# Kernel tuning notes

Hardware: AMD Instinct MI355X
Metric: run time of the kernel (lower is better)

The kernel has to match this reference:

```python
import jax, jax.numpy as jnp
import numpy as np

HID = 32
R = 3
B = 2
IN = 64
N = 100000
E = 1600000
G = 256


def setup_inputs() -> dict:
    key = jax.random.key(0)
    ks = jax.random.split(key, 16)
    x = jax.random.normal(ks[0], (N, IN), dtype=jnp.float32)
    src = jax.random.randint(ks[1], (E,), 0, N)
    dst = jax.random.randint(ks[2], (E,), 0, N)
    etype = jax.random.randint(ks[3], (E,), 0, R)
    graph_ids = jnp.sort(jax.random.randint(ks[4], (N,), 0, G))
    s = 0.05
    basis1 = jax.random.normal(ks[5], (B, IN, HID), dtype=jnp.float32) * s   # layer 1 basis
    basis_r = jax.random.normal(ks[6], (3, B, HID, HID), dtype=jnp.float32) * s  # layers 2-4
    w_comp = jax.random.normal(ks[7], (4, R, B), dtype=jnp.float32) * s     # per-layer basis coeffs
    loop1 = jax.random.normal(ks[8], (IN, HID), dtype=jnp.float32) * s
    loop_r = jax.random.normal(ks[9], (3, HID, HID), dtype=jnp.float32) * s
    bias = jnp.zeros((4, HID), dtype=jnp.float32)
    lin1_w = jax.random.normal(ks[10], (4 * HID, 64), dtype=jnp.float32) * s
    lin1_b = jnp.zeros((64,), dtype=jnp.float32)
    lin2_w = jax.random.normal(ks[11], (64, 1), dtype=jnp.float32) * s
    lin2_b = jnp.zeros((1,), dtype=jnp.float32)
    return dict(x=x, basis1=basis1, basis_r=basis_r, w_comp=w_comp, loop1=loop1,
                loop_r=loop_r, bias=bias, lin1_w=lin1_w, lin1_b=lin1_b,
                lin2_w=lin2_w, lin2_b=lin2_b, src=src, dst=dst, etype=etype,
                graph_ids=graph_ids, num_graphs=G)


def _rel_conv(h, basis, comp, loop_w, b, src, dst, etype, n_nodes):
    # basis-decomposed relation weights: W[r] = sum_b comp[r,b] * basis[b]
    W = jnp.einsum('rb,bio->rio', comp, basis)            # [R, in, out]
    h_rel = jnp.einsum('ni,rio->rno', h, W)               # [R, N, out]
    msg = h_rel[etype, src]                               # [E, out] edge-typed gather
    agg = jax.ops.segment_sum(msg, dst, num_segments=n_nodes)
    return agg + h @ loop_w + b                           # self-loop + bias


def reference(x, basis1, basis_r, w_comp, loop1, loop_r, bias,
              lin1_w, lin1_b, lin2_w, lin2_b,
              src, dst, etype, graph_ids, num_graphs):
    n = x.shape[0]
    h = jnp.tanh(_rel_conv(x, basis1, w_comp[0], loop1, bias[0], src, dst, etype, n))
    states = [h]
    for i in range(3):
        h = jnp.tanh(_rel_conv(h, basis_r[i], w_comp[i + 1], loop_r[i], bias[i + 1],
                               src, dst, etype, n))
        states.append(h)
    feat = jnp.concatenate(states, axis=1)                # [N, 128]
    # mean-pool nodes per graph (diff_pooling ~ dgl mean_nodes)
    summed = jax.ops.segment_sum(feat, graph_ids, num_segments=num_graphs)
    counts = jax.ops.segment_sum(jnp.ones((n,), feat.dtype), graph_ids,
                                 num_segments=num_graphs)
    pooled = summed / jnp.maximum(counts, 1.0)[:, None]   # [G, 128]
    hdn = jax.nn.relu(pooled @ lin1_w + lin1_b)
    out = jax.nn.sigmoid(hdn @ lin2_w + lin2_b)
    return out[:, 0]
```

## Files before the change

### kernel.cpp

```cpp
#include <hip/hip_runtime.h>
#include <cstdint>
#include <cmath>

#define DLO_BITS 7
#define DLO_MASK 127
#define SCAT_Q 2048

__global__ __launch_bounds__(256) void prep_w(
    const float* __restrict__ basis1,
    const float* __restrict__ w_comp,
    const float* __restrict__ loop1,
    float* __restrict__ W)
{
    int tid = blockIdx.x * 256 + threadIdx.x;
    if (tid < 8192) {
        int m = tid >> 11, io = tid & 2047;
        W[tid] = (m < 3)
            ? w_comp[m * 2] * basis1[io] + w_comp[m * 2 + 1] * basis1[2048 + io]
            : loop1[io];
    }
}

__global__ __launch_bounds__(256) void count_kernel(
    const int* __restrict__ dst, int* __restrict__ bcnt, int E, int NB)
{
    __shared__ int cnt[1024];
    for (int i = threadIdx.x; i < NB; i += 256) cnt[i] = 0;
    __syncthreads();
    int base = blockIdx.x * SCAT_Q;
    #pragma unroll
    for (int i = 0; i < SCAT_Q / 256; ++i) {
        int e = base + i * 256 + threadIdx.x;
        if (e < E) atomicAdd(&cnt[dst[e] >> DLO_BITS], 1);
    }
    __syncthreads();
    for (int i = threadIdx.x; i < NB; i += 256)
        if (cnt[i]) atomicAdd(&bcnt[i], cnt[i]);
}

__global__ __launch_bounds__(1024) void scan_kernel(
    const int* __restrict__ bcnt, int* __restrict__ bbase,
    int* __restrict__ bcur, int NB)
{
    __shared__ int s[1024];
    int t = threadIdx.x;
    int v = (t < NB) ? bcnt[t] : 0;
    s[t] = v; __syncthreads();
    for (int off = 1; off < 1024; off <<= 1) {
        int u = (t >= off) ? s[t - off] : 0;
        __syncthreads();
        s[t] += u;
        __syncthreads();
    }
    if (t < NB) { int b = s[t] - v; bbase[t] = b; bcur[t] = b; }
}

__global__ __launch_bounds__(256) void bscatter_kernel(
    const int* __restrict__ src, const int* __restrict__ dst,
    const int* __restrict__ et, int* __restrict__ bcur,
    unsigned* __restrict__ eidx1, int E, int NB)
{
    __shared__ int cnt[1024];
    __shared__ int bbs[1024];
    int tid = threadIdx.x;
    for (int i = tid; i < NB; i += 256) cnt[i] = 0;
    __syncthreads();
    int base = blockIdx.x * SCAT_Q;
    int lim = E - base; if (lim > SCAT_Q) lim = SCAT_Q;
    for (int i = tid; i < lim; i += 256)
        atomicAdd(&cnt[dst[base + i] >> DLO_BITS], 1);
    __syncthreads();
    for (int i = tid; i < NB; i += 256) {
        int c = cnt[i];
        bbs[i] = c ? atomicAdd(&bcur[i], c) : 0;
    }
    __syncthreads();
    for (int i = tid; i < NB; i += 256) cnt[i] = 0;
    __syncthreads();
    for (int i = tid; i < lim; i += 256) {
        int e = base + i;
        int d = dst[e];
        int bk = d >> DLO_BITS;
        int p = bbs[bk] + atomicAdd(&cnt[bk], 1);
        eidx1[p] = (unsigned)src[e] | ((unsigned)et[e] << 17)
                 | ((unsigned)(d & DLO_MASK) << 19);
    }
}

__global__ __launch_bounds__(256) void bucket_sort_kernel(
    const unsigned* __restrict__ eidx1, const int* __restrict__ bbase,
    const int* __restrict__ bcnt, unsigned* __restrict__ eidx2,
    int* __restrict__ rp, int* __restrict__ rend0, int* __restrict__ rend1,
    int* __restrict__ rend, int N)
{
    __shared__ int c512[512], excl[512], w[512];
    int tid = threadIdx.x, b = blockIdx.x;
    int gbase = bbase[b], cnt = bcnt[b], n0 = b << DLO_BITS;
    c512[tid] = 0; c512[tid + 256] = 0;
    __syncthreads();
    for (int k = tid; k < cnt; k += 256) {
        unsigned pk = eidx1[gbase + k];
        int key = (((pk >> 19) & DLO_MASK) << 2) | ((pk >> 17) & 3);
        atomicAdd(&c512[key], 1);
    }
    __syncthreads();
    w[tid] = c512[tid]; w[tid + 256] = c512[tid + 256];
    __syncthreads();
    for (int off = 1; off < 512; off <<= 1) {
        int a1 = (tid >= off) ? w[tid - off] : 0;
        int a2 = (tid + 256 >= off) ? w[tid + 256 - off] : 0;
        __syncthreads();
        w[tid] += a1; w[tid + 256] += a2;
        __syncthreads();
    }
    excl[tid] = w[tid] - c512[tid];
    excl[tid + 256] = w[tid + 256] - c512[tid + 256];
    __syncthreads();
    if (tid < 128) {
        int n = n0 + tid;
        if (n < N) {
            int k0 = tid << 2;
            rp[n]    = gbase + excl[k0];
            rend0[n] = gbase + excl[k0 | 1];
            rend1[n] = gbase + excl[k0 | 2];
            rend[n]  = gbase + excl[k0 | 2] + c512[k0 | 2];
        }
    }
    __syncthreads();
    c512[tid] = 0; c512[tid + 256] = 0;
    __syncthreads();
    for (int k = tid; k < cnt; k += 256) {
        unsigned pk = eidx1[gbase + k];
        int key = (((pk >> 19) & DLO_MASK) << 2) | ((pk >> 17) & 3);
        int p = excl[key] + atomicAdd(&c512[key], 1);
        eidx2[gbase + p] = pk;
    }
}

__global__ __launch_bounds__(256) void dense_kernel(
    const float* __restrict__ x,
    const float* __restrict__ W,
    const float* __restrict__ bias_l,
    float* __restrict__ hrel,
    float* __restrict__ agg,
    int N)
{
    __shared__ float sW[4 * 2048];
    __shared__ float sH[64 * 68];
    const int tid = threadIdx.x;
    for (int i = tid; i < 4 * 2048; i += 256) sW[i] = W[i];
    const int nb = blockIdx.x * 64;
    for (int idx = tid; idx < 64 * 64; idx += 256) {
        int n = idx >> 6, i = idx & 63;
        int gn = nb + n;
        sH[n * 68 + i] = (gn < N) ? x[(size_t)gn * 64 + i] : 0.0f;
    }
    __syncthreads();

    const int m  = tid >> 6;
    const int l  = tid & 63;
    const int ow = l & 7;
    const int ng = l >> 3;

    float acc[8][4];
    #pragma unroll
    for (int j = 0; j < 8; ++j)
        #pragma unroll
        for (int k = 0; k < 4; ++k) acc[j][k] = 0.0f;

    const float* wb = &sW[m * 2048 + ow * 4];
    #pragma unroll 2
    for (int i = 0; i < 64; i += 4) {
        float4 wv0 = *(const float4*)(wb + (i + 0) * 32);
        float4 wv1 = *(const float4*)(wb + (i + 1) * 32);
        float4 wv2 = *(const float4*)(wb + (i + 2) * 32);
        float4 wv3 = *(const float4*)(wb + (i + 3) * 32);
        #pragma unroll
        for (int j = 0; j < 8; ++j) {
            float4 hv = *(const float4*)&sH[(j * 8 + ng) * 68 + i];
            acc[j][0] += hv.x * wv0.x + hv.y * wv1.x + hv.z * wv2.x + hv.w * wv3.x;
            acc[j][1] += hv.x * wv0.y + hv.y * wv1.y + hv.z * wv2.y + hv.w * wv3.y;
            acc[j][2] += hv.x * wv0.z + hv.y * wv1.z + hv.z * wv2.z + hv.w * wv3.z;
            acc[j][3] += hv.x * wv0.w + hv.y * wv1.w + hv.z * wv2.w + hv.w * wv3.w;
        }
    }

    if (m < 3) {
        #pragma unroll
        for (int j = 0; j < 8; ++j) {
            int n = nb + j * 8 + ng;
            if (n < N)
                *(float4*)&hrel[((size_t)m * N + n) * 32 + ow * 4] =
                    make_float4(acc[j][0], acc[j][1], acc[j][2], acc[j][3]);
        }
    } else {
        float4 bb = *(const float4*)&bias_l[ow * 4];
        #pragma unroll
        for (int j = 0; j < 8; ++j) {
            int n = nb + j * 8 + ng;
            if (n < N)
                *(float4*)&agg[(size_t)n * 32 + ow * 4] =
                    make_float4(acc[j][0] + bb.x, acc[j][1] + bb.y,
                                acc[j][2] + bb.z, acc[j][3] + bb.w);
        }
    }
}

__global__ __launch_bounds__(256) void gather1_kernel(
    const unsigned* __restrict__ eidx, const int* __restrict__ rp,
    const int* __restrict__ rend0, const int* __restrict__ rend1,
    const int* __restrict__ rend,
    const float* __restrict__ hrel, const float* __restrict__ agg,
    float* __restrict__ feat, int N)
{
    int tid = blockIdx.x * 256 + threadIdx.x;
    int n = tid >> 3;
    if (n >= N) return;
    int c = (tid & 7) << 2;
    int e0 = rp[n], e1 = rend0[n], e2 = rend1[n], e3 = rend[n];
    const float4 bv = *(const float4*)&agg[(size_t)n * 32 + c];
    float ax = bv.x, ay = bv.y, az = bv.z, aw = bv.w;
    float bx = 0, by = 0, bz = 0, bw = 0;
    #pragma unroll
    for (int seg = 0; seg < 3; ++seg) {
        int ks = (seg == 0) ? e0 : ((seg == 1) ? e1 : e2);
        int ke = (seg == 0) ? e1 : ((seg == 1) ? e2 : e3);
        const float* hb = hrel + (size_t)seg * N * 32 + c;
        int k = ks;
        for (; k + 2 <= ke; k += 2) {
            unsigned p0 = eidx[k], p1 = eidx[k + 1];
            float4 v0 = *(const float4*)&hb[(size_t)(p0 & 0x1FFFF) * 32];
            float4 v1 = *(const float4*)&hb[(size_t)(p1 & 0x1FFFF) * 32];
            ax += v0.x; ay += v0.y; az += v0.z; aw += v0.w;
            bx += v1.x; by += v1.y; bz += v1.z; bw += v1.w;
        }
        if (k < ke) {
            unsigned p = eidx[k];
            float4 v = *(const float4*)&hb[(size_t)(p & 0x1FFFF) * 32];
            ax += v.x; ay += v.y; az += v.z; aw += v.w;
        }
    }
    float4* out = (float4*)&feat[(size_t)n * 128 + c];
    *out = make_float4(tanhf(ax + bx), tanhf(ay + by), tanhf(az + bz), tanhf(aw + bw));
}

__global__ __launch_bounds__(256) void fused_layer_kernel(
    const unsigned* __restrict__ eidx, const int* __restrict__ rp,
    const int* __restrict__ rend0, const int* __restrict__ rend1,
    const int* __restrict__ rend,
    const float* __restrict__ basis_b,
    const float* __restrict__ loop_w,
    const float* __restrict__ bias_l,
    const float* __restrict__ comp,
    const float* __restrict__ feat_in,
    float* __restrict__ feat_out,
    int N)
{
    __shared__ float sB0[1024], sB1[1024], sL[1024];
    __shared__ float sT0[32 * 36], sT1[32 * 36], sH[32 * 36];
    const int tid = threadIdx.x;
    for (int i = tid; i < 1024; i += 256) {
        sB0[i] = basis_b[i];
        sB1[i] = basis_b[1024 + i];
        sL[i]  = loop_w[i];
    }
    const int nn = tid >> 3, cg = (tid & 7) << 2;
    const int n = blockIdx.x * 32 + nn;

    float4 h4 = *(const float4*)&feat_in[(size_t)n * 128 + cg];
    *(float4*)&sH[nn * 36 + cg] = h4;

    int e0 = rp[n], e1 = rend0[n], e2 = rend1[n], e3 = rend[n];
    float t0x = 0, t0y = 0, t0z = 0, t0w = 0;
    float t1x = 0, t1y = 0, t1z = 0, t1w = 0;
    #pragma unroll
    for (int seg = 0; seg < 3; ++seg) {
        int ks = (seg == 0) ? e0 : ((seg == 1) ? e1 : e2);
        int ke = (seg == 0) ? e1 : ((seg == 1) ? e2 : e3);
        float sx = 0, sy = 0, sz = 0, sw = 0;
        float ux = 0, uy = 0, uz = 0, uw = 0;
        int k = ks;
        for (; k + 2 <= ke; k += 2) {
            unsigned p0 = eidx[k], p1 = eidx[k + 1];
            float4 v0 = *(const float4*)&feat_in[(size_t)(p0 & 0x1FFFF) * 128 + cg];
            float4 v1 = *(const float4*)&feat_in[(size_t)(p1 & 0x1FFFF) * 128 + cg];
            sx += v0.x; sy += v0.y; sz += v0.z; sw += v0.w;
            ux += v1.x; uy += v1.y; uz += v1.z; uw += v1.w;
        }
        if (k < ke) {
            unsigned p = eidx[k];
            float4 v = *(const float4*)&feat_in[(size_t)(p & 0x1FFFF) * 128 + cg];
            sx += v.x; sy += v.y; sz += v.z; sw += v.w;
        }
        sx += ux; sy += uy; sz += uz; sw += uw;
        float c0 = comp[seg * 2], c1 = comp[seg * 2 + 1];
        t0x += c0 * sx; t0y += c0 * sy; t0z += c0 * sz; t0w += c0 * sw;
        t1x += c1 * sx; t1y += c1 * sy; t1z += c1 * sz; t1w += c1 * sw;
    }
    *(float4*)&sT0[nn * 36 + cg] = make_float4(t0x, t0y, t0z, t0w);
    *(float4*)&sT1[nn * 36 + cg] = make_float4(t1x, t1y, t1z, t1w);
    __syncthreads();

    float4 bb = *(const float4*)&bias_l[cg];
    float a[4] = {bb.x, bb.y, bb.z, bb.w};
    #pragma unroll 8
    for (int kk = 0; kk < 32; ++kk) {
        float p0 = sT0[nn * 36 + kk];
        float p1 = sT1[nn * 36 + kk];
        float hh = sH[nn * 36 + kk];
        float4 b0 = *(const float4*)&sB0[kk * 32 + cg];
        float4 b1 = *(const float4*)&sB1[kk * 32 + cg];
        float4 lw = *(const float4*)&sL[kk * 32 + cg];
        a[0] += p0 * b0.x + p1 * b1.x + hh * lw.x;
        a[1] += p0 * b0.y + p1 * b1.y + hh * lw.y;
        a[2] += p0 * b0.z + p1 * b1.z + hh * lw.z;
        a[3] += p0 * b0.w + p1 * b1.w + hh * lw.w;
    }
    *(float4*)&feat_out[(size_t)n * 128 + cg] =
        make_float4(tanhf(a[0]), tanhf(a[1]), tanhf(a[2]), tanhf(a[3]));
}

__global__ __launch_bounds__(256) void pool_kernel(
    const float* __restrict__ feat, const int* __restrict__ gid,
    float* __restrict__ pooled, float* __restrict__ cntArr, int N)
{
    int chunk0 = blockIdx.x * 128;
    int ch = threadIdx.x & 127, half = threadIdx.x >> 7;
    int n = chunk0 + half;
    int lim = chunk0 + 128; if (lim > N) lim = N;
    if (n >= lim) return;
    int cur = gid[n];
    float acc = 0.0f; int cc = 0;
    for (; n < lim; n += 2) {
        int g = gid[n];
        if (g != cur) {
            atomicAdd(&pooled[(size_t)cur * 128 + ch], acc);
            if (ch == 0) atomicAdd(&cntArr[cur], (float)cc);
            acc = 0.0f; cc = 0; cur = g;
        }
        acc += feat[(size_t)n * 128 + ch];
        ++cc;
    }
    atomicAdd(&pooled[(size_t)cur * 128 + ch], acc);
    if (ch == 0) atomicAdd(&cntArr[cur], (float)cc);
}

__global__ __launch_bounds__(64) void mlp_kernel(
    const float* __restrict__ pooled, const float* __restrict__ cntArr,
    const float* __restrict__ w1, const float* __restrict__ b1,
    const float* __restrict__ w2, const float* __restrict__ b2,
    float* __restrict__ out)
{
    int g = blockIdx.x;
    int t = threadIdx.x;
    float inv = 1.0f / fmaxf(cntArr[g], 1.0f);
    float acc = b1[t];
    #pragma unroll 8
    for (int k = 0; k < 128; ++k)
        acc += pooled[(size_t)g * 128 + k] * inv * w1[k * 64 + t];
    float h = fmaxf(acc, 0.0f);
    float p = h * w2[t];
    #pragma unroll
    for (int off = 32; off > 0; off >>= 1) p += __shfl_down(p, off, 64);
    if (t == 0) out[g] = 1.0f / (1.0f + expf(-(p + b2[0])));
}

extern "C" void kernel_launch(void* const* d_in, const int* in_sizes, int n_in,
                              void* d_out, int out_size, void* d_ws, size_t ws_size,
                              hipStream_t stream)
{
    const float* x       = (const float*)d_in[0];
    const float* basis1  = (const float*)d_in[1];
    const float* basis_r = (const float*)d_in[2];
    const float* w_comp  = (const float*)d_in[3];
    const float* loop1   = (const float*)d_in[4];
    const float* loop_r  = (const float*)d_in[5];
    const float* bias    = (const float*)d_in[6];
    const float* lin1_w  = (const float*)d_in[7];
    const float* lin1_b  = (const float*)d_in[8];
    const float* lin2_w  = (const float*)d_in[9];
    const float* lin2_b  = (const float*)d_in[10];
    const int*   src     = (const int*)d_in[11];
    const int*   dst     = (const int*)d_in[12];
    const int*   etype   = (const int*)d_in[13];
    const int*   gid     = (const int*)d_in[14];

    const int N = in_sizes[0] / 64;
    const int E = in_sizes[11];
    const int G = out_size;
    const int NB = (N + DLO_MASK) >> DLO_BITS;

    float* ws      = (float*)d_ws;
    float* W       = ws;
    float* hrel    = W + 8192;
    float* agg     = hrel + (size_t)3 * N * 32;
    float* feat    = agg + (size_t)N * 32;
    float* pooled  = feat + (size_t)N * 128;
    float* cntArr  = pooled + (size_t)G * 128;
    int*   bcnt    = (int*)(cntArr + G);
    int*   bbase   = bcnt + NB;
    int*   bcur    = bbase + NB;
    int*   rp      = bcur + NB;
    int*   rend0   = rp + N;
    int*   rend1   = rend0 + N;
    int*   rend    = rend1 + N;
    unsigned* eidx2 = (unsigned*)(rend + N);
    unsigned* eidx1 = (unsigned*)feat;

    hipMemsetAsync(pooled, 0, ((size_t)G * 128 + G + NB) * sizeof(float), stream);
    prep_w<<<32, 256, 0, stream>>>(basis1, w_comp, loop1, W);

    const int nsb = (E + SCAT_Q - 1) / SCAT_Q;
    count_kernel<<<nsb, 256, 0, stream>>>(dst, bcnt, E, NB);
    scan_kernel<<<1, 1024, 0, stream>>>(bcnt, bbase, bcur, NB);
    bscatter_kernel<<<nsb, 256, 0, stream>>>(src, dst, etype, bcur, eidx1, E, NB);
    bucket_sort_kernel<<<NB, 256, 0, stream>>>(eidx1, bbase, bcnt, eidx2,
                                               rp, rend0, rend1, rend, N);

    dense_kernel<<<(N + 63) / 64, 256, 0, stream>>>(x, W, bias, hrel, agg, N);
    gather1_kernel<<<(N * 8 + 255) / 256, 256, 0, stream>>>(
        eidx2, rp, rend0, rend1, rend, hrel, agg, feat, N);

    for (int l = 1; l < 4; ++l) {
        fused_layer_kernel<<<(N + 31) / 32, 256, 0, stream>>>(
            eidx2, rp, rend0, rend1, rend,
            basis_r + (size_t)(l - 1) * 2048,
            loop_r + (size_t)(l - 1) * 1024,
            bias + l * 32,
            w_comp + l * 6,
            feat + (l - 1) * 32,
            feat + l * 32,
            N);
    }

    pool_kernel<<<(N + 127) / 128, 256, 0, stream>>>(feat, gid, pooled, cntArr, N);
    mlp_kernel<<<G, 64, 0, stream>>>(pooled, cntArr, lin1_w, lin1_b, lin2_w, lin2_b, (float*)d_out);
}
```

Before: 360.0 us.

## Replace count+scatter passes with single-pass chunk-local partition and start table

Merges the separate count and global-scatter kernels into one partition kernel. Each block sorts a 4096-edge chunk by bucket in shared memory, writes it contiguously, and records per-chunk bucket start offsets. The bucket sort kernel then gathers each bucket's segments from all chunks using a prefix sum and a binary search. This removes one full pass over the edge arrays and the scattered global writes. In exchange it adds a per-element binary search and scattered reads in the bucket sort.

```diff
diff --git a/kernel.cpp b/kernel.cpp
--- a/kernel.cpp
+++ b/kernel.cpp
@@ -4,7 +4,7 @@
 
 #define DLO_BITS 7
 #define DLO_MASK 127
-#define SCAT_Q 2048
+#define CHUNK 4096
 
 __global__ __launch_bounds__(256) void prep_w(
     const float* __restrict__ basis1,
@@ -21,26 +21,63 @@
     }
 }
 
-__global__ __launch_bounds__(256) void count_kernel(
-    const int* __restrict__ dst, int* __restrict__ bcnt, int E, int NB)
-{
+__global__ __launch_bounds__(256) void part_kernel(
+    const int* __restrict__ src, const int* __restrict__ dst,
+    const int* __restrict__ et, unsigned* __restrict__ eidx1,
+    int* __restrict__ startTab,
+    int* __restrict__ bcnt,
+    int E, int NB)
+{
+    __shared__ unsigned rec[CHUNK];
     __shared__ int cnt[1024];
-    for (int i = threadIdx.x; i < NB; i += 256) cnt[i] = 0;
-    __syncthreads();
-    int base = blockIdx.x * SCAT_Q;
-    #pragma unroll
-    for (int i = 0; i < SCAT_Q / 256; ++i) {
-        int e = base + i * 256 + threadIdx.x;
-        if (e < E) atomicAdd(&cnt[dst[e] >> DLO_BITS], 1);
-    }
-    __syncthreads();
-    for (int i = threadIdx.x; i < NB; i += 256)
-        if (cnt[i]) atomicAdd(&bcnt[i], cnt[i]);
+    __shared__ int w[1024];
+    const int tid = threadIdx.x;
+    const int base = blockIdx.x * CHUNK;
+    int lim = E - base; if (lim > CHUNK) lim = CHUNK;
+
+    cnt[tid] = 0; cnt[tid + 256] = 0; cnt[tid + 512] = 0; cnt[tid + 768] = 0;
+    __syncthreads();
+    for (int i = tid; i < lim; i += 256) {
+        int e = base + i;
+        int d = dst[e];
+        rec[i] = (unsigned)src[e] | ((unsigned)et[e] << 17)
+               | ((unsigned)(d & DLO_MASK) << 19);
+        atomicAdd(&cnt[d >> DLO_BITS], 1);
+    }
+    __syncthreads();
+    w[tid] = cnt[tid]; w[tid + 256] = cnt[tid + 256];
+    w[tid + 512] = cnt[tid + 512]; w[tid + 768] = cnt[tid + 768];
+    __syncthreads();
+    for (int off = 1; off < 1024; off <<= 1) {
+        int a0 = (tid >= off) ? w[tid - off] : 0;
+        int a1 = (tid + 256 >= off) ? w[tid + 256 - off] : 0;
+        int a2 = (tid + 512 >= off) ? w[tid + 512 - off] : 0;
+        int a3 = w[tid + 768 - off];
+        __syncthreads();
+        w[tid] += a0; w[tid + 256] += a1; w[tid + 512] += a2; w[tid + 768] += a3;
+        __syncthreads();
+    }
+    int* st = startTab + blockIdx.x * (NB + 1);
+    for (int bk = tid; bk < NB; bk += 256) {
+        int c = cnt[bk];
+        int ex = w[bk] - c;
+        st[bk] = base + ex;
+        w[bk] = ex;
+        if (c) atomicAdd(&bcnt[bk], c);
+    }
+    if (tid == 0) st[NB] = base + lim;
+    __syncthreads();
+    cnt[tid] = 0; cnt[tid + 256] = 0; cnt[tid + 512] = 0; cnt[tid + 768] = 0;
+    __syncthreads();
+    for (int i = tid; i < lim; i += 256) {
+        int bk = dst[base + i] >> DLO_BITS;
+        int pos = w[bk] + atomicAdd(&cnt[bk], 1);
+        eidx1[base + pos] = rec[i];
+    }
 }
 
 __global__ __launch_bounds__(1024) void scan_kernel(
-    const int* __restrict__ bcnt, int* __restrict__ bbase,
-    int* __restrict__ bcur, int NB)
+    const int* __restrict__ bcnt, int* __restrict__ bbase, int NB)
 {
     __shared__ int s[1024];
     int t = threadIdx.x;
@@ -52,72 +89,63 @@
         s[t] += u;
         __syncthreads();
     }
-    if (t < NB) { int b = s[t] - v; bbase[t] = b; bcur[t] = b; }
-}
-
-__global__ __launch_bounds__(256) void bscatter_kernel(
-    const int* __restrict__ src, const int* __restrict__ dst,
-    const int* __restrict__ et, int* __restrict__ bcur,
-    unsigned* __restrict__ eidx1, int E, int NB)
-{
-    __shared__ int cnt[1024];
-    __shared__ int bbs[1024];
-    int tid = threadIdx.x;
-    for (int i = tid; i < NB; i += 256) cnt[i] = 0;
-    __syncthreads();
-    int base = blockIdx.x * SCAT_Q;
-    int lim = E - base; if (lim > SCAT_Q) lim = SCAT_Q;
-    for (int i = tid; i < lim; i += 256)
-        atomicAdd(&cnt[dst[base + i] >> DLO_BITS], 1);
-    __syncthreads();
-    for (int i = tid; i < NB; i += 256) {
-        int c = cnt[i];
-        bbs[i] = c ? atomicAdd(&bcur[i], c) : 0;
-    }
-    __syncthreads();
-    for (int i = tid; i < NB; i += 256) cnt[i] = 0;
-    __syncthreads();
-    for (int i = tid; i < lim; i += 256) {
-        int e = base + i;
-        int d = dst[e];
-        int bk = d >> DLO_BITS;
-        int p = bbs[bk] + atomicAdd(&cnt[bk], 1);
-        eidx1[p] = (unsigned)src[e] | ((unsigned)et[e] << 17)
-                 | ((unsigned)(d & DLO_MASK) << 19);
-    }
+    if (t < NB) bbase[t] = s[t] - v;
 }
 
 __global__ __launch_bounds__(256) void bucket_sort_kernel(
-    const unsigned* __restrict__ eidx1, const int* __restrict__ bbase,
-    const int* __restrict__ bcnt, unsigned* __restrict__ eidx2,
+    const unsigned* __restrict__ eidx1, const int* __restrict__ startTab,
+    const int* __restrict__ bbase, unsigned* __restrict__ eidx2,
     int* __restrict__ rp, int* __restrict__ rend0, int* __restrict__ rend1,
-    int* __restrict__ rend, int N)
-{
-    __shared__ int c512[512], excl[512], w[512];
-    int tid = threadIdx.x, b = blockIdx.x;
-    int gbase = bbase[b], cnt = bcnt[b], n0 = b << DLO_BITS;
+    int* __restrict__ rend, int N, int NCH, int NB)
+{
+    __shared__ int rbase[512];
+    __shared__ int racc[512];
+    __shared__ int c512[512], excl[512], w2[512];
+    const int tid = threadIdx.x, b = blockIdx.x;
+
+    for (int j = tid; j < 512; j += 256) {
+        int s = 0, len = 0;
+        if (j < NCH) {
+            s = startTab[j * (NB + 1) + b];
+            len = startTab[j * (NB + 1) + b + 1] - s;
+        }
+        rbase[j] = s;
+        racc[j] = len;
+    }
+    __syncthreads();
+    for (int off = 1; off < 512; off <<= 1) {
+        int a1 = (tid >= off) ? racc[tid - off] : 0;
+        int a2 = (tid + 256 >= off) ? racc[tid + 256 - off] : 0;
+        __syncthreads();
+        racc[tid] += a1; racc[tid + 256] += a2;
+        __syncthreads();
+    }
+    const int cnt = racc[NCH - 1];
+    const int gbase = bbase[b];
     c512[tid] = 0; c512[tid + 256] = 0;
     __syncthreads();
-    for (int k = tid; k < cnt; k += 256) {
-        unsigned pk = eidx1[gbase + k];
+    for (int i = tid; i < cnt; i += 256) {
+        int lo = 0, hi = NCH - 1;
+        while (lo < hi) { int mid = (lo + hi) >> 1; if (racc[mid] <= i) lo = mid + 1; else hi = mid; }
+        unsigned pk = eidx1[rbase[lo] + (i - (lo ? racc[lo - 1] : 0))];
         int key = (((pk >> 19) & DLO_MASK) << 2) | ((pk >> 17) & 3);
         atomicAdd(&c512[key], 1);
     }
     __syncthreads();
-    w[tid] = c512[tid]; w[tid + 256] = c512[tid + 256];
+    w2[tid] = c512[tid]; w2[tid + 256] = c512[tid + 256];
     __syncthreads();
     for (int off = 1; off < 512; off <<= 1) {
-        int a1 = (tid >= off) ? w[tid - off] : 0;
-        int a2 = (tid + 256 >= off) ? w[tid + 256 - off] : 0;
-        __syncthreads();
-        w[tid] += a1; w[tid + 256] += a2;
-        __syncthreads();
-    }
-    excl[tid] = w[tid] - c512[tid];
-    excl[tid + 256] = w[tid + 256] - c512[tid + 256];
+        int a1 = (tid >= off) ? w2[tid - off] : 0;
+        int a2 = (tid + 256 >= off) ? w2[tid + 256 - off] : 0;
+        __syncthreads();
+        w2[tid] += a1; w2[tid + 256] += a2;
+        __syncthreads();
+    }
+    excl[tid] = w2[tid] - c512[tid];
+    excl[tid + 256] = w2[tid + 256] - c512[tid + 256];
     __syncthreads();
     if (tid < 128) {
-        int n = n0 + tid;
+        int n = (b << DLO_BITS) + tid;
         if (n < N) {
             int k0 = tid << 2;
             rp[n]    = gbase + excl[k0];
@@ -129,8 +157,10 @@
     __syncthreads();
     c512[tid] = 0; c512[tid + 256] = 0;
     __syncthreads();
-    for (int k = tid; k < cnt; k += 256) {
-        unsigned pk = eidx1[gbase + k];
+    for (int i = tid; i < cnt; i += 256) {
+        int lo = 0, hi = NCH - 1;
+        while (lo < hi) { int mid = (lo + hi) >> 1; if (racc[mid] <= i) lo = mid + 1; else hi = mid; }
+        unsigned pk = eidx1[rbase[lo] + (i - (lo ? racc[lo - 1] : 0))];
         int key = (((pk >> 19) & DLO_MASK) << 2) | ((pk >> 17) & 3);
         int p = excl[key] + atomicAdd(&c512[key], 1);
         eidx2[gbase + p] = pk;
@@ -389,6 +419,7 @@
     const int E = in_sizes[11];
     const int G = out_size;
     const int NB = (N + DLO_MASK) >> DLO_BITS;
+    const int NCH = (E + CHUNK - 1) / CHUNK;
 
     float* ws      = (float*)d_ws;
     float* W       = ws;
@@ -399,23 +430,21 @@
     float* cntArr  = pooled + (size_t)G * 128;
     int*   bcnt    = (int*)(cntArr + G);
     int*   bbase   = bcnt + NB;
-    int*   bcur    = bbase + NB;
-    int*   rp      = bcur + NB;
+    int*   rp      = bbase + NB;
     int*   rend0   = rp + N;
     int*   rend1   = rend0 + N;
     int*   rend    = rend1 + N;
     unsigned* eidx2 = (unsigned*)(rend + N);
     unsigned* eidx1 = (unsigned*)feat;
+    int* startTab  = (int*)feat + (size_t)NCH * CHUNK;
 
     hipMemsetAsync(pooled, 0, ((size_t)G * 128 + G + NB) * sizeof(float), stream);
     prep_w<<<32, 256, 0, stream>>>(basis1, w_comp, loop1, W);
 
-    const int nsb = (E + SCAT_Q - 1) / SCAT_Q;
-    count_kernel<<<nsb, 256, 0, stream>>>(dst, bcnt, E, NB);
-    scan_kernel<<<1, 1024, 0, stream>>>(bcnt, bbase, bcur, NB);
-    bscatter_kernel<<<nsb, 256, 0, stream>>>(src, dst, etype, bcur, eidx1, E, NB);
-    bucket_sort_kernel<<<NB, 256, 0, stream>>>(eidx1, bbase, bcnt, eidx2,
-                                               rp, rend0, rend1, rend, N);
+    part_kernel<<<NCH, 256, 0, stream>>>(src, dst, etype, eidx1, startTab, bcnt, E, NB);
+    scan_kernel<<<1, 1024, 0, stream>>>(bcnt, bbase, NB);
+    bucket_sort_kernel<<<NB, 256, 0, stream>>>(eidx1, startTab, bbase, eidx2,
+                                               rp, rend0, rend1, rend, N, NCH, NB);
 
     dense_kernel<<<(N + 63) / 64, 256, 0, stream>>>(x, W, bias, hrel, agg, N);
     gather1_kernel<<<(N * 8 + 255) / 256, 256, 0, stream>>>(
```

New measurement: 324.6 us. 9.8% less time.
